# Performance work log

Measured on AMD Instinct MI355X. Metric: run time of the kernel, lower is better.

Reference implementation:

```python
import jax, jax.numpy as jnp
import numpy as np

SL, BS, HS = 2048, 2, 1024
FFN, E, TOP_K = 4096, 8, 2


def setup_inputs() -> dict:
    key = jax.random.key(0)
    k1, k2, k3, k4, k5 = jax.random.split(key, 5)
    x = jax.random.normal(k1, (SL, BS, HS), dtype=jnp.float32)
    expert_weights = jax.random.uniform(k2, (SL * BS, TOP_K), dtype=jnp.float32)
    expert_indices = jax.random.randint(k3, (SL * BS, TOP_K), 0, E, dtype=jnp.int32)
    w1 = jax.random.normal(k4, (E, HS, FFN), dtype=jnp.float32) * 0.02
    w2 = jax.random.normal(k5, (E, FFN, HS), dtype=jnp.float32) * 0.02
    return {"x": x, "expert_weights": expert_weights,
            "expert_indices": expert_indices, "w1": w1, "w2": w2}


def reference(x, expert_weights, expert_indices, w1, w2):
    # Dropless MoE: y[t] = sum_k expert_weights[t,k] * MLP_{expert_indices[t,k]}(x[t])
    # Equivalent to megablocks sort/gather/grouped-GEMM/scatter pipeline, expressed
    # as a fixed loop over the (small) expert axis with masked weighted combine.
    sl, bs, hs = x.shape
    xf = x.reshape(-1, hs)                       # [T, hs]
    ew = expert_weights.reshape(xf.shape[0], -1)  # [T, k]
    ei = expert_indices.reshape(xf.shape[0], -1)  # [T, k]
    out = jnp.zeros_like(xf)
    for e in range(w1.shape[0]):
        h = jnp.dot(jax.nn.gelu(jnp.dot(xf, w1[e])), w2[e])   # [T, hs]
        coef = jnp.sum(jnp.where(ei == e, ew, 0.0), axis=-1)  # [T]
        out = out + coef[:, None] * h
    return out.reshape(sl, bs, hs)
```

## Files before the change

kernel.cpp:

```cpp
#include <hip/hip_runtime.h>
#include <stdint.h>

#define SLEN 2048
#define BSZ  2
#define HSZ  1024
#define FFND 4096
#define NEXP 8
#define TOPK 2
#define NTOK (SLEN*BSZ)
#define NSLOT (NTOK*TOPK)

#define BM 128
#define BN 128
#define BK 32
#define STAGE (BM * BK)

#define KSPLIT 2
#define HALFK (FFND / KSPLIT)

using short8 = __attribute__((ext_vector_type(8))) short;
using f32x4  = __attribute__((ext_vector_type(4))) float;

typedef __attribute__((address_space(1))) const unsigned int gu32;
typedef __attribute__((address_space(3))) unsigned int lu32;

__device__ inline void async_copy16(const void* g, void* l){
  __builtin_amdgcn_global_load_lds((gu32*)g, (lu32*)l, 16, 0, 0);
}

__device__ inline unsigned short f2bf(float f){
  unsigned u = __builtin_bit_cast(unsigned, f);
  u += 0x7FFFu + ((u >> 16) & 1u);
  return (unsigned short)(u >> 16);
}

__device__ inline float gelu_tanh(float x){
  float u = 0.7978845608028654f * (x + 0.044715f * x * x * x);
  return 0.5f * x * (1.0f + tanhf(u));
}

__global__ __launch_bounds__(1024) void k_route(const int* __restrict__ ei,
                                                const float* __restrict__ ew,
                                                int* __restrict__ counts,
                                                int* __restrict__ offsets,
                                                int* __restrict__ rowT,
                                                float* __restrict__ rowC){
  __shared__ int hist[NEXP];
  __shared__ int fill[NEXP];
  const int tid = threadIdx.x;
  if (tid < NEXP) hist[tid] = 0;
  __syncthreads();
  int myE[NSLOT / 1024];
  #pragma unroll
  for (int p = 0; p < NSLOT / 1024; p++){
    myE[p] = ei[tid + p * 1024];
    atomicAdd(&hist[myE[p]], 1);
  }
  __syncthreads();
  if (tid == 0){
    int acc = 0;
    for (int e = 0; e < NEXP; e++){
      offsets[e] = acc; counts[e] = hist[e]; fill[e] = acc; acc += hist[e];
    }
  }
  __syncthreads();
  #pragma unroll
  for (int p = 0; p < NSLOT / 1024; p++){
    int i = tid + p * 1024;
    int slot = atomicAdd(&fill[myE[p]], 1);
    rowT[slot] = i >> 1;
    rowC[slot] = ew[i];
  }
}

__global__ void k_gather(const float* __restrict__ x, const int* __restrict__ rowT,
                         unsigned short* __restrict__ Xg){
  int slot = blockIdx.x;
  int t = rowT[slot];
  int c = threadIdx.x * 4;
  float4 v = *(const float4*)(x + (size_t)t * HSZ + c);
  ushort4 o;
  o.x = f2bf(v.x); o.y = f2bf(v.y); o.z = f2bf(v.z); o.w = f2bf(v.w);
  *(ushort4*)(Xg + (size_t)slot * HSZ + c) = o;
}

__global__ __launch_bounds__(256) void k_transpose2(const float* __restrict__ w1,
                                                    const float* __restrict__ w2,
                                                    unsigned short* __restrict__ Wt1,
                                                    unsigned short* __restrict__ Wt2){
  __shared__ unsigned short tile[64][65];
  const int tid = threadIdx.x;
  int z = blockIdx.y;
  const float* src; unsigned short* dst; int R, C, r0, c0;
  if (z < NEXP){
    src = w1 + (size_t)z * HSZ * FFND; dst = Wt1 + (size_t)z * HSZ * FFND;
    R = HSZ; C = FFND;
    c0 = (blockIdx.x & 63) * 64; r0 = (blockIdx.x >> 6) * 64;
  } else {
    z -= NEXP;
    src = w2 + (size_t)z * FFND * HSZ; dst = Wt2 + (size_t)z * FFND * HSZ;
    R = FFND; C = HSZ;
    c0 = (blockIdx.x & 15) * 64; r0 = (blockIdx.x >> 4) * 64;
  }
  #pragma unroll
  for (int p = 0; p < 4; p++){
    int r  = p * 16 + (tid >> 4);
    int cc = (tid & 15) * 4;
    float4 v = *(const float4*)(src + (size_t)(r0 + r) * C + c0 + cc);
    tile[r][cc]   = f2bf(v.x);
    tile[r][cc+1] = f2bf(v.y);
    tile[r][cc+2] = f2bf(v.z);
    tile[r][cc+3] = f2bf(v.w);
  }
  __syncthreads();
  #pragma unroll
  for (int p = 0; p < 4; p++){
    int c  = p * 16 + (tid >> 4);
    int rr = (tid & 15) * 4;
    ushort4 o;
    o.x = tile[rr][c]; o.y = tile[rr+1][c]; o.z = tile[rr+2][c]; o.w = tile[rr+3][c];
    *(ushort4*)(dst + (size_t)(c0 + c) * R + r0 + rr) = o;
  }
}

__device__ inline void gemm_core(const unsigned short* __restrict__ Ag, int lda, int rows,
                                 const unsigned short* __restrict__ Bg, int ldb, int K,
                                 unsigned short* As, unsigned short* Bs,
                                 f32x4 acc[4][4])
{
  const int tid  = threadIdx.x;
  const int lane = tid & 63;
  const int wid  = tid >> 6;
  const int wm   = (wid & 1) * 64;
  const int wn   = (wid >> 1) * 64;
  const int q    = lane >> 4;
  const int l16  = lane & 15;

  auto stage = [&](int k0, int s){
    #pragma unroll
    for (int p = 0; p < 2; p++){
      int c  = (wid * 2 + p) * 64 + lane;
      int r  = c >> 2;
      int kp = (c & 3) * 8;
      int ra = min(r, rows - 1);
      async_copy16(Ag + (size_t)ra * lda + k0 + kp, As + s * STAGE + (wid * 2 + p) * 512);
      async_copy16(Bg + (size_t)r  * ldb + k0 + kp, Bs + s * STAGE + (wid * 2 + p) * 512);
    }
  };

  const int niter = K / BK;
  stage(0, 0);
  for (int k = 0; k < niter; k++){
    __syncthreads();
    if (k + 1 < niter) stage((k + 1) * BK, (k + 1) & 1);
    const unsigned short* Ak = As + (k & 1) * STAGE;
    const unsigned short* Bk = Bs + (k & 1) * STAGE;

    short8 af[4], bfr[4];
    #pragma unroll
    for (int i = 0; i < 4; i++)
      af[i] = *(const short8*)(Ak + (wm + i * 16 + l16) * BK + q * 8);
    #pragma unroll
    for (int j = 0; j < 4; j++)
      bfr[j] = *(const short8*)(Bk + (wn + j * 16 + l16) * BK + q * 8);

    #pragma unroll
    for (int i = 0; i < 4; i++)
      #pragma unroll
      for (int j = 0; j < 4; j++)
        acc[i][j] = __builtin_amdgcn_mfma_f32_16x16x32_bf16(af[i], bfr[j], acc[i][j], 0, 0, 0);
  }
}

__global__ __launch_bounds__(256) void k_gemm1(const unsigned short* __restrict__ Xg,
                                               const unsigned short* __restrict__ Wt1,
                                               unsigned short* __restrict__ H,
                                               const int* __restrict__ counts,
                                               const int* __restrict__ offsets)
{
  __shared__ unsigned short smem[4 * STAGE];
  unsigned short* As = smem;
  unsigned short* Bs = smem + 2 * STAGE;
  const int e    = blockIdx.z;
  const int cnt  = counts[e];
  const int mblk = blockIdx.y;
  if (mblk * BM >= cnt) return;
  const int n0   = blockIdx.x * BN;
  const int row0 = offsets[e] + mblk * BM;
  const int rows = min(BM, cnt - mblk * BM);

  f32x4 acc[4][4] = {};
  gemm_core(Xg + (size_t)row0 * HSZ, HSZ, rows,
            Wt1 + (size_t)e * HSZ * FFND + (size_t)n0 * HSZ, HSZ, HSZ, As, Bs, acc);
  __syncthreads();

  const int lane = threadIdx.x & 63, wid = threadIdx.x >> 6;
  const int wm = (wid & 1) * 64, wn = (wid >> 1) * 64;
  const int q = lane >> 4, l16 = lane & 15;

  unsigned short* scr = smem + wid * (16 * 68);
  #pragma unroll
  for (int i = 0; i < 4; i++){
    #pragma unroll
    for (int j = 0; j < 4; j++)
      #pragma unroll
      for (int r = 0; r < 4; r++)
        scr[(q * 4 + r) * 68 + j * 16 + l16] = f2bf(gelu_tanh(acc[i][j][r]));
    #pragma unroll
    for (int p = 0; p < 2; p++){
      int rr = p * 8 + (lane >> 3);
      int cc = (lane & 7) * 8;
      short8 v = *(const short8*)(scr + rr * 68 + cc);
      int grow = wm + i * 16 + rr;
      if (grow < rows)
        *(short8*)(H + (size_t)(row0 + grow) * FFND + n0 + wn + cc) = v;
    }
  }
}

__global__ __launch_bounds__(256) void k_gemm2(const unsigned short* __restrict__ H,
                                               const unsigned short* __restrict__ Wt2,
                                               float* __restrict__ out,
                                               const int* __restrict__ counts,
                                               const int* __restrict__ offsets,
                                               const int* __restrict__ rowT,
                                               const float* __restrict__ rowC)
{
  __shared__ unsigned short smem[4 * STAGE];
  unsigned short* As = smem;
  unsigned short* Bs = smem + 2 * STAGE;
  const int e    = blockIdx.z;
  const int cnt  = counts[e];
  const int ks   = blockIdx.y % KSPLIT;
  const int mblk = blockIdx.y / KSPLIT;
  if (mblk * BM >= cnt) return;
  const int n0   = blockIdx.x * BN;
  const int row0 = offsets[e] + mblk * BM;
  const int rows = min(BM, cnt - mblk * BM);

  f32x4 acc[4][4] = {};
  gemm_core(H + (size_t)row0 * FFND + ks * HALFK, FFND, rows,
            Wt2 + (size_t)e * FFND * HSZ + (size_t)n0 * FFND + ks * HALFK, FFND,
            HALFK, As, Bs, acc);

  const int lane = threadIdx.x & 63, wid = threadIdx.x >> 6;
  const int wm = (wid & 1) * 64, wn = (wid >> 1) * 64;
  const int q = lane >> 4, l16 = lane & 15;
  #pragma unroll
  for (int i = 0; i < 4; i++)
    #pragma unroll
    for (int r = 0; r < 4; r++){
      int row = wm + i * 16 + q * 4 + r;
      if (row < rows){
        int g = row0 + row;
        float cf = rowC[g];
        float* op = out + (size_t)rowT[g] * HSZ + n0 + wn;
        #pragma unroll
        for (int j = 0; j < 4; j++)
          atomicAdd(op + j * 16 + l16, cf * acc[i][j][r]);
      }
    }
}

static inline size_t align_up(size_t v, size_t a){ return (v + a - 1) & ~(a - 1); }

extern "C" void kernel_launch(void* const* d_in, const int* in_sizes, int n_in,
                              void* d_out, int out_size, void* d_ws, size_t ws_size,
                              hipStream_t stream) {
  const float* x  = (const float*)d_in[0];
  const float* ew = (const float*)d_in[1];
  const int*   ei = (const int*)d_in[2];
  const float* w1 = (const float*)d_in[3];
  const float* w2 = (const float*)d_in[4];
  float* out = (float*)d_out;

  char* base = (char*)d_ws;
  size_t off = 0;
  int* counts  = (int*)(base + off); off += 64;
  int* offsets = (int*)(base + off); off = align_up(off + 64, 4096);
  int* rowT    = (int*)(base + off); off += (size_t)NSLOT * 4;
  float* rowC  = (float*)(base + off); off = align_up(off + (size_t)NSLOT * 4, 1 << 20);
  unsigned short* Xg  = (unsigned short*)(base + off); off = align_up(off + (size_t)NSLOT * HSZ * 2, 1 << 20);
  unsigned short* H   = (unsigned short*)(base + off); off = align_up(off + (size_t)NSLOT * FFND * 2, 1 << 20);
  unsigned short* Wt1 = (unsigned short*)(base + off); off = align_up(off + (size_t)NEXP * HSZ * FFND * 2, 1 << 20);
  unsigned short* Wt2 = (unsigned short*)(base + off); off += (size_t)NEXP * FFND * HSZ * 2;
  (void)ws_size;

  hipMemsetAsync(d_out, 0, (size_t)out_size * sizeof(float), stream);

  k_route <<<1, 1024, 0, stream>>>(ei, ew, counts, offsets, rowT, rowC);
  k_gather<<<NSLOT, 256, 0, stream>>>(x, rowT, Xg);

  k_transpose2<<<dim3(1024, 2 * NEXP), 256, 0, stream>>>(w1, w2, Wt1, Wt2);

  k_gemm1<<<dim3(FFND / BN, 64, NEXP), 256, 0, stream>>>(Xg, Wt1, H, counts, offsets);
  k_gemm2<<<dim3(HSZ / BN, 64 * KSPLIT, NEXP), 256, 0, stream>>>(H, Wt2, out, counts, offsets, rowT, rowC);
}
```

Before: 618.2 us.

## Rewrite expert GEMMs with 256x256 tiles, swizzled LDS and 4-stage pipeline

Replaces the 128x128x32 double-buffered GEMM core with a 256x256x64 tile run by 512 threads (8 waves). The new core uses XOR-swizzled LDS layout, a four-slab ring of async global-to-LDS copies with explicit vmcnt waits, phased A/B loads interleaved with MFMA issue, and raised wave priority around the MFMA block. The goal is more operand reuse per loaded byte, fewer LDS bank conflicts and better overlap of loads with math in both expert GEMMs. The costs are a 128 KB LDS footprint per block, higher register pressure from 8x4 accumulators, and more wasted work in partially filled row tiles.

```diff
diff --git a/kernel.cpp b/kernel.cpp
--- a/kernel.cpp
+++ b/kernel.cpp
@@ -10,11 +10,9 @@
 #define NTOK (SLEN*BSZ)
 #define NSLOT (NTOK*TOPK)
 
-#define BM 128
-#define BN 128
-#define BK 32
-#define STAGE (BM * BK)
-
+#define BM2 256
+#define BN2 256
+#define BK2 64
 #define KSPLIT 2
 #define HALFK (FFND / KSPLIT)
 
@@ -123,84 +121,126 @@
   }
 }
 
-__device__ inline void gemm_core(const unsigned short* __restrict__ Ag, int lda, int rows,
-                                 const unsigned short* __restrict__ Bg, int ldb, int K,
-                                 unsigned short* As, unsigned short* Bs,
-                                 f32x4 acc[4][4])
+__device__ __forceinline__ void gemm_core256(
+    const unsigned short* __restrict__ Ag, int lda, int rows,
+    const unsigned short* __restrict__ Bg, int ldb, int K,
+    unsigned short* smem, f32x4 acc[8][4])
 {
   const int tid  = threadIdx.x;
   const int lane = tid & 63;
   const int wid  = tid >> 6;
-  const int wm   = (wid & 1) * 64;
-  const int wn   = (wid >> 1) * 64;
+  const int wr   = wid >> 2;
+  const int wc   = wid & 3;
   const int q    = lane >> 4;
   const int l16  = lane & 15;
 
-  auto stage = [&](int k0, int s){
-    #pragma unroll
-    for (int p = 0; p < 2; p++){
-      int c  = (wid * 2 + p) * 64 + lane;
-      int r  = c >> 2;
-      int kp = (c & 3) * 8;
-      int ra = min(r, rows - 1);
-      async_copy16(Ag + (size_t)ra * lda + k0 + kp, As + s * STAGE + (wid * 2 + p) * 512);
-      async_copy16(Bg + (size_t)r  * ldb + k0 + kp, Bs + s * STAGE + (wid * 2 + p) * 512);
-    }
-  };
-
-  const int niter = K / BK;
-  stage(0, 0);
-  for (int k = 0; k < niter; k++){
-    __syncthreads();
-    if (k + 1 < niter) stage((k + 1) * BK, (k + 1) & 1);
-    const unsigned short* Ak = As + (k & 1) * STAGE;
-    const unsigned short* Bk = Bs + (k & 1) * STAGE;
-
-    short8 af[4], bfr[4];
-    #pragma unroll
-    for (int i = 0; i < 4; i++)
-      af[i] = *(const short8*)(Ak + (wm + i * 16 + l16) * BK + q * 8);
-    #pragma unroll
-    for (int j = 0; j < 4; j++)
-      bfr[j] = *(const short8*)(Bk + (wn + j * 16 + l16) * BK + q * 8);
-
-    #pragma unroll
-    for (int i = 0; i < 4; i++)
+  char* smemc = (char*)smem;
+
+  const int srow = wid * 16 + (lane >> 2);
+  const int sx   = (lane & 3) ^ (srow & 3);
+  const char* A8 = (const char*)Ag;
+  const char* B8 = (const char*)Bg;
+  unsigned ao0 = (unsigned)(min(srow,       rows - 1) * lda) * 2u + (unsigned)(sx << 4);
+  unsigned ao1 = (unsigned)(min(srow + 128, rows - 1) * lda) * 2u + (unsigned)(sx << 4);
+  unsigned bo0 = (unsigned)( srow        * ldb) * 2u + (unsigned)(sx << 4);
+  unsigned bo1 = (unsigned)((srow + 128) * ldb) * 2u + (unsigned)(sx << 4);
+  char* ldsA = smemc + wid * 1024;
+  char* ldsB = smemc + 65536 + wid * 1024;
+
+  const int rxs = ((q ^ (lane & 3)) << 4);
+  const unsigned rbA = (unsigned)((wr * 128 + l16) * 64 + rxs);
+  const unsigned rbB = (unsigned)((wc * 64  + l16) * 64 + rxs);
+
+  short8 bf[4];
+
+  async_copy16(A8 + ao0,      ldsA);
+  async_copy16(A8 + ao1,      ldsA + 8192);
+  async_copy16(B8 + bo0,      ldsB);
+  async_copy16(B8 + bo1,      ldsB + 8192);
+  async_copy16(A8 + ao0 + 64, ldsA + 16384);
+  async_copy16(A8 + ao1 + 64, ldsA + 16384 + 8192);
+  async_copy16(B8 + bo0 + 64, ldsB + 16384);
+  async_copy16(B8 + bo1 + 64, ldsB + 16384 + 8192);
+  ao0 += 128; ao1 += 128; bo0 += 128; bo1 += 128;
+
+  const int T = K / BK2;
+
+  auto phase = [&](int ks, int ih, int sRd, int sW, int stA){
+    if (ih == 0) asm volatile("s_waitcnt vmcnt(4)" ::: "memory");
+    __builtin_amdgcn_s_barrier();
+    asm volatile("" ::: "memory");
+    const char* aslab = smemc + sRd * 16384;
+    const char* bslab = smemc + 65536 + sRd * 16384;
+    if (ih == 0){
       #pragma unroll
       for (int j = 0; j < 4; j++)
-        acc[i][j] = __builtin_amdgcn_mfma_f32_16x16x32_bf16(af[i], bfr[j], acc[i][j], 0, 0, 0);
-  }
-}
-
-__global__ __launch_bounds__(256) void k_gemm1(const unsigned short* __restrict__ Xg,
-                                               const unsigned short* __restrict__ Wt1,
-                                               unsigned short* __restrict__ H,
-                                               const int* __restrict__ counts,
-                                               const int* __restrict__ offsets)
+        bf[j] = *(const short8*)(bslab + rbB + j * 1024);
+    }
+    short8 af[4];
+    #pragma unroll
+    for (int ii = 0; ii < 4; ii++)
+      af[ii] = *(const short8*)(aslab + rbA + (ih * 4 + ii) * 1024);
+    const unsigned kb = (unsigned)(ks << 6);
+    if (stA){
+      async_copy16(A8 + (ao0 + kb), ldsA + sW * 16384);
+      async_copy16(A8 + (ao1 + kb), ldsA + sW * 16384 + 8192);
+    } else {
+      async_copy16(B8 + (bo0 + kb), ldsB + sW * 16384);
+      async_copy16(B8 + (bo1 + kb), ldsB + sW * 16384 + 8192);
+    }
+    __builtin_amdgcn_s_setprio(1);
+    #pragma unroll
+    for (int ii = 0; ii < 4; ii++)
+      #pragma unroll
+      for (int j = 0; j < 4; j++)
+        acc[ih*4+ii][j] = __builtin_amdgcn_mfma_f32_16x16x32_bf16(af[ii], bf[j], acc[ih*4+ii][j], 0, 0, 0);
+    __builtin_amdgcn_s_setprio(0);
+  };
+
+  for (int t = 0; t < T; t += 2){
+    phase(0, 0, 0, 2, 1);
+    phase(0, 1, 0, 2, 0);
+    phase(1, 0, 1, 3, 1);
+    phase(1, 1, 1, 3, 0);
+    if (t + 3 <= T){ ao0 += 128; ao1 += 128; bo0 += 128; bo1 += 128; }
+    phase(0, 0, 2, 0, 1);
+    phase(0, 1, 2, 0, 0);
+    phase(1, 0, 3, 1, 1);
+    phase(1, 1, 3, 1, 0);
+    if (t + 4 <= T){ ao0 += 128; ao1 += 128; bo0 += 128; bo1 += 128; }
+  }
+  asm volatile("s_waitcnt vmcnt(0)" ::: "memory");
+  __builtin_amdgcn_s_barrier();
+  asm volatile("" ::: "memory");
+}
+
+__global__ __launch_bounds__(512, 2) void k_gemm1(const unsigned short* __restrict__ Xg,
+                                                  const unsigned short* __restrict__ Wt1,
+                                                  unsigned short* __restrict__ H,
+                                                  const int* __restrict__ counts,
+                                                  const int* __restrict__ offsets)
 {
-  __shared__ unsigned short smem[4 * STAGE];
-  unsigned short* As = smem;
-  unsigned short* Bs = smem + 2 * STAGE;
+  __shared__ unsigned short smem[65536];
   const int e    = blockIdx.z;
   const int cnt  = counts[e];
   const int mblk = blockIdx.y;
-  if (mblk * BM >= cnt) return;
-  const int n0   = blockIdx.x * BN;
-  const int row0 = offsets[e] + mblk * BM;
-  const int rows = min(BM, cnt - mblk * BM);
-
-  f32x4 acc[4][4] = {};
-  gemm_core(Xg + (size_t)row0 * HSZ, HSZ, rows,
-            Wt1 + (size_t)e * HSZ * FFND + (size_t)n0 * HSZ, HSZ, HSZ, As, Bs, acc);
-  __syncthreads();
+  if (mblk * BM2 >= cnt) return;
+  const int n0   = blockIdx.x * BN2;
+  const int row0 = offsets[e] + mblk * BM2;
+  const int rows = min(BM2, cnt - mblk * BM2);
+
+  f32x4 acc[8][4] = {};
+  gemm_core256(Xg + (size_t)row0 * HSZ, HSZ, rows,
+               Wt1 + (size_t)e * HSZ * FFND + (size_t)n0 * HSZ, HSZ, HSZ,
+               smem, acc);
 
   const int lane = threadIdx.x & 63, wid = threadIdx.x >> 6;
-  const int wm = (wid & 1) * 64, wn = (wid >> 1) * 64;
+  const int wr = wid >> 2, wc = wid & 3;
   const int q = lane >> 4, l16 = lane & 15;
 
   unsigned short* scr = smem + wid * (16 * 68);
   #pragma unroll
-  for (int i = 0; i < 4; i++){
+  for (int i = 0; i < 8; i++){
     #pragma unroll
     for (int j = 0; j < 4; j++)
       #pragma unroll
@@ -211,50 +251,48 @@
       int rr = p * 8 + (lane >> 3);
       int cc = (lane & 7) * 8;
       short8 v = *(const short8*)(scr + rr * 68 + cc);
-      int grow = wm + i * 16 + rr;
+      int grow = wr * 128 + i * 16 + rr;
       if (grow < rows)
-        *(short8*)(H + (size_t)(row0 + grow) * FFND + n0 + wn + cc) = v;
-    }
-  }
-}
-
-__global__ __launch_bounds__(256) void k_gemm2(const unsigned short* __restrict__ H,
-                                               const unsigned short* __restrict__ Wt2,
-                                               float* __restrict__ out,
-                                               const int* __restrict__ counts,
-                                               const int* __restrict__ offsets,
-                                               const int* __restrict__ rowT,
-                                               const float* __restrict__ rowC)
+        *(short8*)(H + (size_t)(row0 + grow) * FFND + n0 + wc * 64 + cc) = v;
+    }
+  }
+}
+
+__global__ __launch_bounds__(512, 2) void k_gemm2(const unsigned short* __restrict__ H,
+                                                  const unsigned short* __restrict__ Wt2,
+                                                  float* __restrict__ out,
+                                                  const int* __restrict__ counts,
+                                                  const int* __restrict__ offsets,
+                                                  const int* __restrict__ rowT,
+                                                  const float* __restrict__ rowC)
 {
-  __shared__ unsigned short smem[4 * STAGE];
-  unsigned short* As = smem;
-  unsigned short* Bs = smem + 2 * STAGE;
+  __shared__ unsigned short smem[65536];
   const int e    = blockIdx.z;
   const int cnt  = counts[e];
-  const int ks   = blockIdx.y % KSPLIT;
-  const int mblk = blockIdx.y / KSPLIT;
-  if (mblk * BM >= cnt) return;
-  const int n0   = blockIdx.x * BN;
-  const int row0 = offsets[e] + mblk * BM;
-  const int rows = min(BM, cnt - mblk * BM);
-
-  f32x4 acc[4][4] = {};
-  gemm_core(H + (size_t)row0 * FFND + ks * HALFK, FFND, rows,
-            Wt2 + (size_t)e * FFND * HSZ + (size_t)n0 * FFND + ks * HALFK, FFND,
-            HALFK, As, Bs, acc);
+  const int ks2  = blockIdx.y & 1;
+  const int mblk = blockIdx.y >> 1;
+  if (mblk * BM2 >= cnt) return;
+  const int n0   = blockIdx.x * BN2;
+  const int row0 = offsets[e] + mblk * BM2;
+  const int rows = min(BM2, cnt - mblk * BM2);
+
+  f32x4 acc[8][4] = {};
+  gemm_core256(H + (size_t)row0 * FFND + ks2 * HALFK, FFND, rows,
+               Wt2 + (size_t)e * FFND * HSZ + (size_t)n0 * FFND + ks2 * HALFK, FFND,
+               HALFK, smem, acc);
 
   const int lane = threadIdx.x & 63, wid = threadIdx.x >> 6;
-  const int wm = (wid & 1) * 64, wn = (wid >> 1) * 64;
+  const int wr = wid >> 2, wc = wid & 3;
   const int q = lane >> 4, l16 = lane & 15;
   #pragma unroll
-  for (int i = 0; i < 4; i++)
+  for (int i = 0; i < 8; i++)
     #pragma unroll
     for (int r = 0; r < 4; r++){
-      int row = wm + i * 16 + q * 4 + r;
+      int row = wr * 128 + i * 16 + q * 4 + r;
       if (row < rows){
         int g = row0 + row;
         float cf = rowC[g];
-        float* op = out + (size_t)rowT[g] * HSZ + n0 + wn;
+        float* op = out + (size_t)rowT[g] * HSZ + n0 + wc * 64;
         #pragma unroll
         for (int j = 0; j < 4; j++)
           atomicAdd(op + j * 16 + l16, cf * acc[i][j][r]);
@@ -293,6 +331,6 @@
 
   k_transpose2<<<dim3(1024, 2 * NEXP), 256, 0, stream>>>(w1, w2, Wt1, Wt2);
 
-  k_gemm1<<<dim3(FFND / BN, 64, NEXP), 256, 0, stream>>>(Xg, Wt1, H, counts, offsets);
-  k_gemm2<<<dim3(HSZ / BN, 64 * KSPLIT, NEXP), 256, 0, stream>>>(H, Wt2, out, counts, offsets, rowT, rowC);
-}
+  k_gemm1<<<dim3(FFND / BN2, 32, NEXP), 512, 0, stream>>>(Xg, Wt1, H, counts, offsets);
+  k_gemm2<<<dim3(HSZ / BN2, 32 * KSPLIT, NEXP), 512, 0, stream>>>(H, Wt2, out, counts, offsets, rowT, rowC);
+}
```

Result: no change. 622.0 us (+0.6%).
